# Kernel tuning notes

Measured on AMD Instinct MI355X. Metric: run time of the kernel, lower is better.

Reference implementation:

```python
import jax, jax.numpy as jnp
import numpy as np

N_NODES = 100000
N_EDGES = 1600000
IN_DIM, HID_DIM, OUT_DIM = 128, 64, 128


def setup_inputs() -> dict:
    key = jax.random.key(0)
    k1, k2, k3, k4 = jax.random.split(key, 4)
    x = jax.random.normal(k1, (N_NODES, IN_DIM), dtype=jnp.float32)
    edge_index = jax.random.randint(k2, (2, N_EDGES), 0, N_NODES, dtype=jnp.int32)
    W_conv = jax.random.normal(k3, (IN_DIM, HID_DIM), dtype=jnp.float32) * (1.0 / np.sqrt(IN_DIM))
    b_conv = jnp.zeros((HID_DIM,), dtype=jnp.float32)
    W_lin = jax.random.normal(k4, (HID_DIM, OUT_DIM), dtype=jnp.float32) * (1.0 / np.sqrt(HID_DIM))
    b_lin = jnp.zeros((OUT_DIM,), dtype=jnp.float32)
    return {"x": x, "edge_index": edge_index, "W_conv": W_conv, "b_conv": b_conv,
            "W_lin": W_lin, "b_lin": b_lin}


def gcn_conv(x, edge_index, W, b):
    """PyG GCNConv: linear transform, symmetric-normalized aggregation with self-loops, bias."""
    n = x.shape[0]
    loop = jnp.arange(n, dtype=edge_index.dtype)
    src = jnp.concatenate([edge_index[0], loop])  # message sources (x_j)
    dst = jnp.concatenate([edge_index[1], loop])  # aggregation targets
    # degree of target nodes (counting self-loops), D^{-1/2}
    deg = jax.ops.segment_sum(jnp.ones_like(dst, dtype=x.dtype), dst, num_segments=n)
    dinv = jnp.where(deg > 0, jax.lax.rsqrt(deg), 0.0)
    norm = dinv[src] * dinv[dst]  # [E+N]
    h = x @ W  # [N, hid]
    msg = h[src] * norm[:, None]  # gather + normalize, [E+N, hid]
    agg = jax.ops.segment_sum(msg, dst, num_segments=n)  # scatter-add
    return agg + b


def reference(x, edge_index, W_conv, b_conv, W_lin, b_lin):
    h = gcn_conv(x, edge_index, W_conv, b_conv)
    h = jax.nn.relu(h)
    return h @ W_lin + b_lin
```

## Files before the change

kernel.cpp:

```cpp
#include <hip/hip_runtime.h>
#include <hip/hip_bf16.h>

#define NN 100000
#define NE 1600000
#define NBUK 782
#define NBLK 400
#define CHUNK 4000
#define NGB 1563

typedef unsigned short ushort_t;
typedef __bf16 bf16x8 __attribute__((ext_vector_type(8)));
typedef float  f32x4  __attribute__((ext_vector_type(4)));

static __device__ __forceinline__ float bf2f(unsigned u) {
    union { unsigned i; float f; } c; c.i = u << 16; return c.f;
}
static __device__ __forceinline__ float bf2f_hi(unsigned u) {
    union { unsigned i; float f; } c; c.i = u & 0xffff0000u; return c.f;
}
static __device__ __forceinline__ ushort_t f2bf(float f) {
    union { __hip_bfloat16 b; ushort_t u; } c; c.b = __float2bfloat16(f); return c.u;
}

__global__ __launch_bounds__(256) void k_part_hist(const int* __restrict__ dst,
                                                   int* __restrict__ bhist) {
    __shared__ int h[NBUK];
    int t = threadIdx.x, b = blockIdx.x;
    for (int i = t; i < NBUK; i += 256) h[i] = 0;
    __syncthreads();
    int e0 = b * CHUNK;
    for (int r = 0; r < CHUNK; r += 256)
        if (r + t < CHUNK) atomicAdd(&h[dst[e0 + r + t] >> 7], 1);
    __syncthreads();
    for (int i = t; i < NBUK; i += 256) bhist[b * NBUK + i] = h[i];
}

__global__ __launch_bounds__(512) void k_colscan(const int* __restrict__ bhist,
                                                 int* __restrict__ base_excl,
                                                 int* __restrict__ coltot) {
    __shared__ int s[512];
    int k = blockIdx.x, t = threadIdx.x;
    int v = (t < NBLK) ? bhist[t * NBUK + k] : 0;
    s[t] = v;
    __syncthreads();
#pragma unroll
    for (int o = 1; o < 512; o <<= 1) {
        int x = (t >= o) ? s[t - o] : 0;
        __syncthreads();
        s[t] += x;
        __syncthreads();
    }
    if (t < NBLK) base_excl[t * NBUK + k] = s[t] - v;
    if (t == 511) coltot[k] = s[511];
}

__global__ __launch_bounds__(1024) void k_scanb2(const int* __restrict__ coltot,
                                                 int* __restrict__ bstart,
                                                 int* __restrict__ bcnt) {
    __shared__ int s[1024];
    int t = threadIdx.x;
    int v = (t < NBUK) ? coltot[t] : 0;
    s[t] = v;
    __syncthreads();
#pragma unroll
    for (int o = 1; o < 1024; o <<= 1) {
        int x = (t >= o) ? s[t - o] : 0;
        __syncthreads();
        s[t] += x;
        __syncthreads();
    }
    if (t < NBUK) { bstart[t] = s[t] - v; bcnt[t] = v; }
}

__global__ __launch_bounds__(256) void k_scatter2(const int* __restrict__ ei,
                                                  const int* __restrict__ bstart,
                                                  const int* __restrict__ base_excl,
                                                  unsigned* __restrict__ ebuf) {
    __shared__ int cur[NBUK];
    int t = threadIdx.x, b = blockIdx.x;
    for (int i = t; i < NBUK; i += 256) cur[i] = 0;
    __syncthreads();
    int e0 = b * CHUNK;
    for (int r = 0; r < CHUNK; r += 256) {
        if (r + t < CHUNK) {
            int e = e0 + r + t;
            int sv = ei[e];
            int dv = ei[NE + e];
            int k = dv >> 7;
            int rk = atomicAdd(&cur[k], 1);
            int pos = bstart[k] + base_excl[b * NBUK + k] + rk;
            ebuf[pos] = (unsigned)sv | ((unsigned)(dv & 127) << 17);
        }
    }
}

__global__ __launch_bounds__(256) void k_sort(const int* __restrict__ bstart,
                                              const int* __restrict__ bcnt,
                                              const unsigned* __restrict__ ebuf,
                                              int* __restrict__ csr,
                                              int* __restrict__ offsets,
                                              int* __restrict__ deg,
                                              float* __restrict__ dinv) {
    __shared__ int hist[128];
    __shared__ int off[128];
    __shared__ int cur[128];
    int t = threadIdx.x, b = blockIdx.x;
    if (t < 128) hist[t] = 0;
    __syncthreads();
    int base = bstart[b], ne = bcnt[b];
    for (int i = t; i < ne; i += 256) atomicAdd(&hist[ebuf[base + i] >> 17], 1);
    __syncthreads();
    if (t < 128) off[t] = hist[t];
    __syncthreads();
#pragma unroll
    for (int o = 1; o < 128; o <<= 1) {
        int x = 0;
        if (t < 128 && t >= o) x = off[t - o];
        __syncthreads();
        if (t < 128) off[t] += x;
        __syncthreads();
    }
    if (t < 128) {
        int excl = off[t] - hist[t];
        cur[t] = excl;
        int node = b * 128 + t;
        if (node < NN) {
            offsets[node] = base + excl;
            deg[node]     = hist[t];
            dinv[node]    = rsqrtf((float)(hist[t] + 1));
        }
    }
    __syncthreads();
    for (int i = t; i < ne; i += 256) {
        unsigned pe = ebuf[base + i];
        int dl = pe >> 17;
        int pos = atomicAdd(&cur[dl], 1);
        csr[base + pos] = (int)(pe & 0x1FFFF);
    }
}

__global__ __launch_bounds__(256) void k_wprep(const float* __restrict__ Wc,
                                               const float* __restrict__ Wl,
                                               ushort_t* __restrict__ wtb,
                                               ushort_t* __restrict__ w2tb) {
    int t = blockIdx.x * 256 + threadIdx.x;
    int d = t & 63, k = t >> 6;
    wtb[d * 128 + k] = f2bf(Wc[t]);
    int j = t & 127, k2 = t >> 7;
    w2tb[j * 64 + k2] = f2bf(Wl[t]);
}

__global__ __launch_bounds__(256) void k_gemm1(const float* __restrict__ x,
                                               const ushort_t* __restrict__ wtb,
                                               const float* __restrict__ dinv,
                                               ushort_t* __restrict__ hp) {
    int t = threadIdx.x;
    int w = t >> 6, lane = t & 63, l15 = lane & 15, quad = lane >> 4;
    int gn = blockIdx.x * 64 + w * 16 + l15;
    int gnc = gn < NN ? gn : NN - 1;
    const float*    xp = x   + (size_t)gnc * 128 + quad * 8;
    const ushort_t* wp = wtb + l15 * 128 + quad * 8;
    f32x4 acc[4];
#pragma unroll
    for (int dt = 0; dt < 4; ++dt) { acc[dt][0]=0.f; acc[dt][1]=0.f; acc[dt][2]=0.f; acc[dt][3]=0.f; }

#pragma unroll
    for (int kt = 0; kt < 4; ++kt) {
        float4 v0 = *(const float4*)(xp + kt * 32);
        float4 v1 = *(const float4*)(xp + kt * 32 + 4);
        union { ushort_t u[8]; bf16x8 v; } cv;
        cv.u[0]=f2bf(v0.x); cv.u[1]=f2bf(v0.y); cv.u[2]=f2bf(v0.z); cv.u[3]=f2bf(v0.w);
        cv.u[4]=f2bf(v1.x); cv.u[5]=f2bf(v1.y); cv.u[6]=f2bf(v1.z); cv.u[7]=f2bf(v1.w);
        bf16x8 bv = cv.v;
#pragma unroll
        for (int dt = 0; dt < 4; ++dt) {
            bf16x8 av = *(const bf16x8*)(wp + dt * 16 * 128 + kt * 32);
            acc[dt] = __builtin_amdgcn_mfma_f32_16x16x32_bf16(av, bv, acc[dt], 0, 0, 0);
        }
    }
    if (gn < NN) {
        float dv = dinv[gn];
#pragma unroll
        for (int dt = 0; dt < 4; ++dt) {
            uint2 o;
            o.x = (unsigned)f2bf(dv * acc[dt][0]) | ((unsigned)f2bf(dv * acc[dt][1]) << 16);
            o.y = (unsigned)f2bf(dv * acc[dt][2]) | ((unsigned)f2bf(dv * acc[dt][3]) << 16);
            *(uint2*)&hp[(size_t)gn * 64 + dt * 16 + quad * 4] = o;
        }
    }
}

__global__ __launch_bounds__(256) void k_gather(const int* __restrict__ offsets,
                                                const int* __restrict__ deg,
                                                const int* __restrict__ csr,
                                                const float* __restrict__ dinv,
                                                const ushort_t* __restrict__ hp,
                                                const float* __restrict__ b_conv,
                                                ushort_t* __restrict__ a) {
    int node = __builtin_amdgcn_readfirstlane((blockIdx.x * 256 + threadIdx.x) >> 6);
    int lane = threadIdx.x & 63;
    int g   = lane >> 4;
    int l16 = lane & 15;
    int start = offsets[node];
    int cnt   = deg[node];
    const ushort_t* hpc = hp + l16 * 4;

    float s0 = 0.f, s1 = 0.f, s2 = 0.f, s3 = 0.f;
#pragma unroll 1
    for (int j0 = 0; j0 < cnt; j0 += 64) {
        int m = cnt - j0; m = m < 64 ? m : 64;
        int col = 0;
        if (lane < m) col = csr[start + j0 + lane];
#pragma unroll 2
        for (int jj = 0; jj < m; jj += 16) {
            int e0 = jj + g, e1 = jj + 4 + g, e2 = jj + 8 + g, e3 = jj + 12 + g;
            int c0 = __shfl(col, e0, 64);
            int c1 = __shfl(col, e1, 64);
            int c2 = __shfl(col, e2, 64);
            int c3 = __shfl(col, e3, 64);
            uint2 d0 = *(const uint2*)(hpc + (size_t)c0 * 64);
            uint2 d1 = *(const uint2*)(hpc + (size_t)c1 * 64);
            uint2 d2 = *(const uint2*)(hpc + (size_t)c2 * 64);
            uint2 d3 = *(const uint2*)(hpc + (size_t)c3 * 64);
            if (e0 >= m) { d0.x = 0u; d0.y = 0u; }
            if (e1 >= m) { d1.x = 0u; d1.y = 0u; }
            if (e2 >= m) { d2.x = 0u; d2.y = 0u; }
            if (e3 >= m) { d3.x = 0u; d3.y = 0u; }
            s0 += bf2f(d0.x);    s1 += bf2f_hi(d0.x);
            s2 += bf2f(d0.y);    s3 += bf2f_hi(d0.y);
            s0 += bf2f(d1.x);    s1 += bf2f_hi(d1.x);
            s2 += bf2f(d1.y);    s3 += bf2f_hi(d1.y);
            s0 += bf2f(d2.x);    s1 += bf2f_hi(d2.x);
            s2 += bf2f(d2.y);    s3 += bf2f_hi(d2.y);
            s0 += bf2f(d3.x);    s1 += bf2f_hi(d3.x);
            s2 += bf2f(d3.y);    s3 += bf2f_hi(d3.y);
        }
    }
    s0 += __shfl_xor(s0, 16, 64); s1 += __shfl_xor(s1, 16, 64);
    s2 += __shfl_xor(s2, 16, 64); s3 += __shfl_xor(s3, 16, 64);
    s0 += __shfl_xor(s0, 32, 64); s1 += __shfl_xor(s1, 32, 64);
    s2 += __shfl_xor(s2, 32, 64); s3 += __shfl_xor(s3, 32, 64);

    uint2 sl = *(const uint2*)(hpc + (size_t)node * 64);
    s0 += bf2f(sl.x); s1 += bf2f_hi(sl.x); s2 += bf2f(sl.y); s3 += bf2f_hi(sl.y);
    float dv = dinv[node];
    float4 bc = *(const float4*)(b_conv + l16 * 4);
    float v0 = fmaxf(dv * s0 + bc.x, 0.f);
    float v1 = fmaxf(dv * s1 + bc.y, 0.f);
    float v2 = fmaxf(dv * s2 + bc.z, 0.f);
    float v3 = fmaxf(dv * s3 + bc.w, 0.f);
    if (lane < 16) {
        uint2 o;
        o.x = (unsigned)f2bf(v0) | ((unsigned)f2bf(v1) << 16);
        o.y = (unsigned)f2bf(v2) | ((unsigned)f2bf(v3) << 16);
        *(uint2*)&a[(size_t)node * 64 + l16 * 4] = o;
    }
}

__global__ __launch_bounds__(256) void k_epi(const ushort_t* __restrict__ a,
                                             const ushort_t* __restrict__ w2tb,
                                             const float* __restrict__ blin,
                                             float* __restrict__ out) {
    int t = threadIdx.x;
    int w = t >> 6, lane = t & 63, l15 = lane & 15, quad = lane >> 4;
    int gn = blockIdx.x * 64 + w * 16 + l15;
    int gnc = gn < NN ? gn : NN - 1;
    const ushort_t* ap = a    + (size_t)gnc * 64 + quad * 8;
    const ushort_t* wp = w2tb + l15 * 64 + quad * 8;
    f32x4 acc[8];
#pragma unroll
    for (int jt = 0; jt < 8; ++jt) { acc[jt][0]=0.f; acc[jt][1]=0.f; acc[jt][2]=0.f; acc[jt][3]=0.f; }

#pragma unroll
    for (int kt = 0; kt < 2; ++kt) {
        bf16x8 bv = *(const bf16x8*)(ap + kt * 32);
#pragma unroll
        for (int jt = 0; jt < 8; ++jt) {
            bf16x8 av = *(const bf16x8*)(wp + jt * 16 * 64 + kt * 32);
            acc[jt] = __builtin_amdgcn_mfma_f32_16x16x32_bf16(av, bv, acc[jt], 0, 0, 0);
        }
    }
    if (gn < NN) {
#pragma unroll
        for (int jt = 0; jt < 8; ++jt) {
            int j0 = jt * 16 + quad * 4;
            float4 b4 = *(const float4*)(blin + j0);
            float4 o;
            o.x = acc[jt][0] + b4.x; o.y = acc[jt][1] + b4.y;
            o.z = acc[jt][2] + b4.z; o.w = acc[jt][3] + b4.w;
            *(float4*)&out[(size_t)gn * 128 + j0] = o;
        }
    }
}

extern "C" void kernel_launch(void* const* d_in, const int* in_sizes, int n_in,
                              void* d_out, int out_size, void* d_ws, size_t ws_size,
                              hipStream_t stream) {
    const float* x  = (const float*)d_in[0];
    const int*   ei = (const int*)d_in[1];
    const float* Wc = (const float*)d_in[2];
    const float* bc = (const float*)d_in[3];
    const float* Wl = (const float*)d_in[4];
    const float* bl = (const float*)d_in[5];
    float* out = (float*)d_out;

    char* ws = (char*)d_ws;
    int*      bhist     = (int*)(ws + 0);
    int*      base_excl = (int*)(ws + 1251200);
    int*      coltot    = (int*)(ws + 2502400);
    int*      bstart    = (int*)(ws + 2505600);
    int*      bcnt      = (int*)(ws + 2508800);
    int*      offsets   = (int*)(ws + 2512000);
    int*      deg       = (int*)(ws + 2912384);
    float*    dinv      = (float*)(ws + 3312768);
    unsigned* ebuf      = (unsigned*)(ws + 3713152);
    int*      csr       = (int*)(ws + 10113152);
    ushort_t* hp        = (ushort_t*)(ws + 16513152);
    ushort_t* a         = (ushort_t*)(ws + 29313152);
    ushort_t* wtb  = (ushort_t*)(ws + 3713152);
    ushort_t* w2tb = wtb + 8192;

    k_part_hist<<<NBLK, 256, 0, stream>>>(ei + NE, bhist);
    k_colscan <<<NBUK, 512, 0, stream>>>(bhist, base_excl, coltot);
    k_scanb2  <<<1, 1024, 0, stream>>>(coltot, bstart, bcnt);
    k_scatter2<<<NBLK, 256, 0, stream>>>(ei, bstart, base_excl, ebuf);
    k_sort    <<<NBUK, 256, 0, stream>>>(bstart, bcnt, ebuf, csr, offsets, deg, dinv);
    k_wprep   <<<32, 256, 0, stream>>>(Wc, Wl, wtb, w2tb);
    k_gemm1   <<<NGB, 256, 0, stream>>>(x, wtb, dinv, hp);
    k_gather  <<<NN * 64 / 256, 256, 0, stream>>>(offsets, deg, csr, dinv, hp, bc, a);
    k_epi     <<<NGB, 256, 0, stream>>>(a, w2tb, bl, out);
}
```

Baseline: 235.6 us.

## Gather four nodes per wave, widen partition grid, fuse weight prep into histogram

After: 235.1 us. No clear change (-0.3%).

```diff
diff --git a/kernel.cpp b/kernel.cpp
--- a/kernel.cpp
+++ b/kernel.cpp
@@ -4,8 +4,8 @@
 #define NN 100000
 #define NE 1600000
 #define NBUK 782
-#define NBLK 400
-#define CHUNK 4000
+#define NBLK 1600
+#define CHUNK 1000
 #define NGB 1563
 
 typedef unsigned short ushort_t;
@@ -22,15 +22,27 @@
     union { __hip_bfloat16 b; ushort_t u; } c; c.b = __float2bfloat16(f); return c.u;
 }
 
-__global__ __launch_bounds__(256) void k_part_hist(const int* __restrict__ dst,
-                                                   int* __restrict__ bhist) {
+__global__ __launch_bounds__(256) void k_pre(const int* __restrict__ ei,
+                                             const float* __restrict__ Wc,
+                                             const float* __restrict__ Wl,
+                                             int* __restrict__ bhist,
+                                             ushort_t* __restrict__ wtb,
+                                             ushort_t* __restrict__ w2tb) {
+    int b = blockIdx.x, t = threadIdx.x;
+    if (b >= NBLK) {
+        int i = (b - NBLK) * 256 + t;
+        int d = i & 63, k = i >> 6;
+        wtb[d * 128 + k] = f2bf(Wc[i]);
+        int j = i & 127, k2 = i >> 7;
+        w2tb[j * 64 + k2] = f2bf(Wl[i]);
+        return;
+    }
     __shared__ int h[NBUK];
-    int t = threadIdx.x, b = blockIdx.x;
     for (int i = t; i < NBUK; i += 256) h[i] = 0;
     __syncthreads();
+    const int* dst = ei + NE;
     int e0 = b * CHUNK;
-    for (int r = 0; r < CHUNK; r += 256)
-        if (r + t < CHUNK) atomicAdd(&h[dst[e0 + r + t] >> 7], 1);
+    for (int r = t; r < CHUNK; r += 256) atomicAdd(&h[dst[e0 + r] >> 7], 1);
     __syncthreads();
     for (int i = t; i < NBUK; i += 256) bhist[b * NBUK + i] = h[i];
 }
@@ -40,8 +52,15 @@
                                                  int* __restrict__ coltot) {
     __shared__ int s[512];
     int k = blockIdx.x, t = threadIdx.x;
-    int v = (t < NBLK) ? bhist[t * NBUK + k] : 0;
-    s[t] = v;
+    int v0 = 0, v1 = 0, v2 = 0, v3 = 0;
+    if (t < 400) {
+        v0 = bhist[(4 * t + 0) * NBUK + k];
+        v1 = bhist[(4 * t + 1) * NBUK + k];
+        v2 = bhist[(4 * t + 2) * NBUK + k];
+        v3 = bhist[(4 * t + 3) * NBUK + k];
+    }
+    int tsum = v0 + v1 + v2 + v3;
+    s[t] = tsum;
     __syncthreads();
 #pragma unroll
     for (int o = 1; o < 512; o <<= 1) {
@@ -50,7 +69,13 @@
         s[t] += x;
         __syncthreads();
     }
-    if (t < NBLK) base_excl[t * NBUK + k] = s[t] - v;
+    if (t < 400) {
+        int excl = s[t] - tsum;
+        base_excl[(4 * t + 0) * NBUK + k] = excl;
+        base_excl[(4 * t + 1) * NBUK + k] = excl + v0;
+        base_excl[(4 * t + 2) * NBUK + k] = excl + v0 + v1;
+        base_excl[(4 * t + 3) * NBUK + k] = excl + v0 + v1 + v2;
+    }
     if (t == 511) coltot[k] = s[511];
 }
 
@@ -81,16 +106,14 @@
     for (int i = t; i < NBUK; i += 256) cur[i] = 0;
     __syncthreads();
     int e0 = b * CHUNK;
-    for (int r = 0; r < CHUNK; r += 256) {
-        if (r + t < CHUNK) {
-            int e = e0 + r + t;
-            int sv = ei[e];
-            int dv = ei[NE + e];
-            int k = dv >> 7;
-            int rk = atomicAdd(&cur[k], 1);
-            int pos = bstart[k] + base_excl[b * NBUK + k] + rk;
-            ebuf[pos] = (unsigned)sv | ((unsigned)(dv & 127) << 17);
-        }
+    for (int r = t; r < CHUNK; r += 256) {
+        int e = e0 + r;
+        int sv = ei[e];
+        int dv = ei[NE + e];
+        int k = dv >> 7;
+        int rk = atomicAdd(&cur[k], 1);
+        int pos = bstart[k] + base_excl[b * NBUK + k] + rk;
+        ebuf[pos] = (unsigned)sv | ((unsigned)(dv & 127) << 17);
     }
 }
 
@@ -139,17 +162,6 @@
     }
 }
 
-__global__ __launch_bounds__(256) void k_wprep(const float* __restrict__ Wc,
-                                               const float* __restrict__ Wl,
-                                               ushort_t* __restrict__ wtb,
-                                               ushort_t* __restrict__ w2tb) {
-    int t = blockIdx.x * 256 + threadIdx.x;
-    int d = t & 63, k = t >> 6;
-    wtb[d * 128 + k] = f2bf(Wc[t]);
-    int j = t & 127, k2 = t >> 7;
-    w2tb[j * 64 + k2] = f2bf(Wl[t]);
-}
-
 __global__ __launch_bounds__(256) void k_gemm1(const float* __restrict__ x,
                                                const ushort_t* __restrict__ wtb,
                                                const float* __restrict__ dinv,
@@ -197,50 +209,44 @@
                                                 const ushort_t* __restrict__ hp,
                                                 const float* __restrict__ b_conv,
                                                 ushort_t* __restrict__ a) {
-    int node = __builtin_amdgcn_readfirstlane((blockIdx.x * 256 + threadIdx.x) >> 6);
-    int lane = threadIdx.x & 63;
-    int g   = lane >> 4;
-    int l16 = lane & 15;
+    int t = threadIdx.x;
+    int lane = t & 63;
+    int g = lane >> 4, l16 = lane & 15;
+    int wave = (blockIdx.x * 256 + t) >> 6;
+    int node = wave * 4 + g;
     int start = offsets[node];
     int cnt   = deg[node];
     const ushort_t* hpc = hp + l16 * 4;
 
+    int cmax = cnt;
+    { int o1 = __shfl_xor(cmax, 16, 64); cmax = cmax > o1 ? cmax : o1;
+      int o2 = __shfl_xor(cmax, 32, 64); cmax = cmax > o2 ? cmax : o2; }
+
     float s0 = 0.f, s1 = 0.f, s2 = 0.f, s3 = 0.f;
 #pragma unroll 1
-    for (int j0 = 0; j0 < cnt; j0 += 64) {
-        int m = cnt - j0; m = m < 64 ? m : 64;
+    for (int j0 = 0; j0 < cmax; j0 += 16) {
         int col = 0;
-        if (lane < m) col = csr[start + j0 + lane];
-#pragma unroll 2
-        for (int jj = 0; jj < m; jj += 16) {
-            int e0 = jj + g, e1 = jj + 4 + g, e2 = jj + 8 + g, e3 = jj + 12 + g;
-            int c0 = __shfl(col, e0, 64);
-            int c1 = __shfl(col, e1, 64);
-            int c2 = __shfl(col, e2, 64);
-            int c3 = __shfl(col, e3, 64);
-            uint2 d0 = *(const uint2*)(hpc + (size_t)c0 * 64);
-            uint2 d1 = *(const uint2*)(hpc + (size_t)c1 * 64);
-            uint2 d2 = *(const uint2*)(hpc + (size_t)c2 * 64);
-            uint2 d3 = *(const uint2*)(hpc + (size_t)c3 * 64);
-            if (e0 >= m) { d0.x = 0u; d0.y = 0u; }
-            if (e1 >= m) { d1.x = 0u; d1.y = 0u; }
-            if (e2 >= m) { d2.x = 0u; d2.y = 0u; }
-            if (e3 >= m) { d3.x = 0u; d3.y = 0u; }
-            s0 += bf2f(d0.x);    s1 += bf2f_hi(d0.x);
-            s2 += bf2f(d0.y);    s3 += bf2f_hi(d0.y);
-            s0 += bf2f(d1.x);    s1 += bf2f_hi(d1.x);
-            s2 += bf2f(d1.y);    s3 += bf2f_hi(d1.y);
-            s0 += bf2f(d2.x);    s1 += bf2f_hi(d2.x);
-            s2 += bf2f(d2.y);    s3 += bf2f_hi(d2.y);
-            s0 += bf2f(d3.x);    s1 += bf2f_hi(d3.x);
-            s2 += bf2f(d3.y);    s3 += bf2f_hi(d3.y);
-        }
-    }
-    s0 += __shfl_xor(s0, 16, 64); s1 += __shfl_xor(s1, 16, 64);
-    s2 += __shfl_xor(s2, 16, 64); s3 += __shfl_xor(s3, 16, 64);
-    s0 += __shfl_xor(s0, 32, 64); s1 += __shfl_xor(s1, 32, 64);
-    s2 += __shfl_xor(s2, 32, 64); s3 += __shfl_xor(s3, 32, 64);
-
+        if (j0 + l16 < cnt) col = csr[start + j0 + l16];
+        int mg = cnt - j0;
+#pragma unroll
+        for (int jj = 0; jj < 16; jj += 8) {
+            int cc[8]; uint2 dd[8];
+#pragma unroll
+            for (int u = 0; u < 8; ++u)
+                cc[u] = __shfl(col, (lane & 48) + jj + u, 64);
+#pragma unroll
+            for (int u = 0; u < 8; ++u) {
+                int c = (jj + u < mg) ? cc[u] : node;
+                dd[u] = *(const uint2*)(hpc + (size_t)c * 64);
+            }
+#pragma unroll
+            for (int u = 0; u < 8; ++u) {
+                if (jj + u >= mg) { dd[u].x = 0u; dd[u].y = 0u; }
+                s0 += bf2f(dd[u].x); s1 += bf2f_hi(dd[u].x);
+                s2 += bf2f(dd[u].y); s3 += bf2f_hi(dd[u].y);
+            }
+        }
+    }
     uint2 sl = *(const uint2*)(hpc + (size_t)node * 64);
     s0 += bf2f(sl.x); s1 += bf2f_hi(sl.x); s2 += bf2f(sl.y); s3 += bf2f_hi(sl.y);
     float dv = dinv[node];
@@ -249,12 +255,10 @@
     float v1 = fmaxf(dv * s1 + bc.y, 0.f);
     float v2 = fmaxf(dv * s2 + bc.z, 0.f);
     float v3 = fmaxf(dv * s3 + bc.w, 0.f);
-    if (lane < 16) {
-        uint2 o;
-        o.x = (unsigned)f2bf(v0) | ((unsigned)f2bf(v1) << 16);
-        o.y = (unsigned)f2bf(v2) | ((unsigned)f2bf(v3) << 16);
-        *(uint2*)&a[(size_t)node * 64 + l16 * 4] = o;
-    }
+    uint2 o;
+    o.x = (unsigned)f2bf(v0) | ((unsigned)f2bf(v1) << 16);
+    o.y = (unsigned)f2bf(v2) | ((unsigned)f2bf(v3) << 16);
+    *(uint2*)&a[(size_t)node * 64 + l16 * 4] = o;
 }
 
 __global__ __launch_bounds__(256) void k_epi(const ushort_t* __restrict__ a,
@@ -306,27 +310,26 @@
 
     char* ws = (char*)d_ws;
     int*      bhist     = (int*)(ws + 0);
-    int*      base_excl = (int*)(ws + 1251200);
-    int*      coltot    = (int*)(ws + 2502400);
-    int*      bstart    = (int*)(ws + 2505600);
-    int*      bcnt      = (int*)(ws + 2508800);
-    int*      offsets   = (int*)(ws + 2512000);
-    int*      deg       = (int*)(ws + 2912384);
-    float*    dinv      = (float*)(ws + 3312768);
-    unsigned* ebuf      = (unsigned*)(ws + 3713152);
-    int*      csr       = (int*)(ws + 10113152);
-    ushort_t* hp        = (ushort_t*)(ws + 16513152);
-    ushort_t* a         = (ushort_t*)(ws + 29313152);
-    ushort_t* wtb  = (ushort_t*)(ws + 3713152);
-    ushort_t* w2tb = wtb + 8192;
-
-    k_part_hist<<<NBLK, 256, 0, stream>>>(ei + NE, bhist);
+    int*      base_excl = (int*)(ws + 5004800);
+    int*      coltot    = (int*)(ws + 10009600);
+    int*      bstart    = (int*)(ws + 10012800);
+    int*      bcnt      = (int*)(ws + 10016000);
+    int*      offsets   = (int*)(ws + 10019200);
+    int*      deg       = (int*)(ws + 10419584);
+    float*    dinv      = (float*)(ws + 10819968);
+    ushort_t* wtb       = (ushort_t*)(ws + 11220352);
+    ushort_t* w2tb      = (ushort_t*)(ws + 11236736);
+    unsigned* ebuf      = (unsigned*)(ws + 11253120);
+    int*      csr       = (int*)(ws + 17653120);
+    ushort_t* hp        = (ushort_t*)(ws + 24053120);
+    ushort_t* a         = (ushort_t*)(ws + 36853120);
+
+    k_pre     <<<NBLK + 32, 256, 0, stream>>>(ei, Wc, Wl, bhist, wtb, w2tb);
     k_colscan <<<NBUK, 512, 0, stream>>>(bhist, base_excl, coltot);
     k_scanb2  <<<1, 1024, 0, stream>>>(coltot, bstart, bcnt);
     k_scatter2<<<NBLK, 256, 0, stream>>>(ei, bstart, base_excl, ebuf);
     k_sort    <<<NBUK, 256, 0, stream>>>(bstart, bcnt, ebuf, csr, offsets, deg, dinv);
-    k_wprep   <<<32, 256, 0, stream>>>(Wc, Wl, wtb, w2tb);
     k_gemm1   <<<NGB, 256, 0, stream>>>(x, wtb, dinv, hp);
-    k_gather  <<<NN * 64 / 256, 256, 0, stream>>>(offsets, deg, csr, dinv, hp, bc, a);
+    k_gather  <<<NN / 16, 256, 0, stream>>>(offsets, deg, csr, dinv, hp, bc, a);
     k_epi     <<<NGB, 256, 0, stream>>>(a, w2tb, bl, out);
 }
```
